# Kernel optimization log

Measured on AMD Instinct MI355X. Metric: run time of the kernel, lower is better.

The kernel has to match this reference:

```python
import jax, jax.numpy as jnp
import numpy as np

D_IN = 512
HLS = [1024, 1024, 512]
N_Q = 4096
N_K = 16384
N_CLASSES = 100
BN_EPS = 1e-5


def _bn(x, gamma, beta):
    # BatchNorm1d in training mode: per-batch mean/biased-var normalization
    m = jnp.mean(x, axis=0)
    v = jnp.var(x, axis=0)
    return gamma * (x - m) * jax.lax.rsqrt(v + BN_EPS) + beta


def _neg_cdist(a, b):
    # -||a_i - b_j||_2 via expanded form (GEMM-dominated)
    a2 = jnp.sum(a * a, axis=1, keepdims=True)          # [N,1]
    b2 = jnp.sum(b * b, axis=1, keepdims=True).T        # [1,M]
    d2 = a2 + b2 - 2.0 * (a @ b.T)                      # [N,M]
    return -jnp.sqrt(jnp.maximum(d2, 0.0))


def setup_inputs() -> dict:
    key = jax.random.key(0)
    ks = jax.random.split(key, 32)
    inp = {
        "x": jax.random.normal(ks[0], (N_Q, D_IN), jnp.float32),
        "x_n": jax.random.normal(ks[1], (N_K, D_IN), jnp.float32),
        "y_n": jax.random.randint(ks[2], (N_K,), 0, N_CLASSES, jnp.int32),
        "in_gamma": jnp.ones((D_IN,), jnp.float32),
        "in_beta": jnp.zeros((D_IN,), jnp.float32),
    }
    dims = [D_IN] + HLS
    ki = 3
    for i in range(len(HLS)):
        fan_in = dims[i]
        bound = 1.0 / np.sqrt(fan_in)
        inp[f"W{i}"] = jax.random.uniform(ks[ki], (dims[i + 1], dims[i]), jnp.float32, -bound, bound); ki += 1
        inp[f"b{i}"] = jax.random.uniform(ks[ki], (dims[i + 1],), jnp.float32, -bound, bound); ki += 1
        inp[f"g{i}"] = jnp.ones((dims[i + 1],), jnp.float32)
        inp[f"bt{i}"] = jnp.zeros((dims[i + 1],), jnp.float32)
    return inp


def reference(x, x_n, y_n, in_gamma, in_beta,
              W0, b0, g0, bt0, W1, b1, g1, bt1, W2, b2, g2, bt2):
    x = _bn(x, in_gamma, in_beta)
    x_n = _bn(x_n, in_gamma, in_beta)
    layers = [(W0, b0, g0, bt0), (W1, b1, g1, bt1), (W2, b2, g2, bt2)]
    for W, b, g, bt in layers:
        x = _bn(jnp.tanh(x @ W.T + b), g, bt)
        x_n = _bn(jnp.tanh(x_n @ W.T + b), g, bt)
    sim = _neg_cdist(x, x_n)                       # [N_Q, N_K]
    scores = jax.nn.softmax(sim, axis=1)
    y_ohe = jax.nn.one_hot(y_n, N_CLASSES, dtype=x.dtype)  # [N_K, C]
    return jnp.clip(scores @ y_ohe, 0.0, 1.0)
```

## Files before the change

kernel.cpp:

```cpp
#include <hip/hip_runtime.h>
#include <math.h>

#define NQ 4096
#define NK 16384
#define NROWS 20480
#define NCLS 100
#define PCLS 112
#define DCH 16

typedef __attribute__((ext_vector_type(8))) short bf16x8;
typedef __attribute__((ext_vector_type(4))) float f32x4;

__device__ inline unsigned short f2bf(float f) {
  unsigned u = __float_as_uint(f);
  u += 0x7fff + ((u >> 16) & 1);
  return (unsigned short)(u >> 16);
}
__device__ inline void upk(unsigned u, float& a, float& b) {
  a = __uint_as_float(u << 16);
  b = __uint_as_float(u & 0xffff0000u);
}
__device__ inline float fast_tanh(float x) {
  float e = __expf(2.f * x);
  return 1.f - 2.f / (e + 1.f);
}
__device__ inline void gload_lds16(const unsigned short* g, unsigned short* l) {
  __builtin_amdgcn_global_load_lds(
      (const __attribute__((address_space(1))) unsigned int*)g,
      (__attribute__((address_space(3))) unsigned int*)l, 16, 0, 0);
}

__global__ __launch_bounds__(256) void conv_bf16(
    const float* __restrict__ in, unsigned short* __restrict__ outp, size_t n4) {
  size_t i = (size_t)blockIdx.x * 256 + threadIdx.x;
  size_t stride = (size_t)gridDim.x * 256;
  for (; i < n4; i += stride) {
    float4 v = ((const float4*)in)[i];
    unsigned lo = (unsigned)f2bf(v.x) | ((unsigned)f2bf(v.y) << 16);
    unsigned hi = (unsigned)f2bf(v.z) | ((unsigned)f2bf(v.w) << 16);
    ((uint2*)outp)[i] = make_uint2(lo, hi);
  }
}

__global__ __launch_bounds__(256) void colstats_part_f(
    const float* __restrict__ A, int D, int rpc, float* __restrict__ part) {
  int j = blockIdx.x * 256 + threadIdx.x;
  int c = blockIdx.y;
  const float* p = A + (size_t)c * rpc * D + j;
  float s = 0.f, s2 = 0.f;
#pragma unroll 4
  for (int r = 0; r < rpc; ++r) {
    float v = p[(size_t)r * D];
    s += v; s2 += v * v;
  }
  part[(size_t)c * 2 * D + j] = s;
  part[(size_t)c * 2 * D + D + j] = s2;
}

__global__ __launch_bounds__(256) void finish_ab(
    const float* __restrict__ part, int D, float invN,
    const float* __restrict__ g, const float* __restrict__ bt,
    float* __restrict__ ab) {
  int j = blockIdx.x * 256 + threadIdx.x;
  if (j >= D) return;
  float s = 0.f, s2 = 0.f;
  for (int c = 0; c < 64; ++c) {
    s += part[(size_t)c * 2 * D + j];
    s2 += part[(size_t)c * 2 * D + D + j];
  }
  float m = s * invN;
  float v = fmaxf(s2 * invN - m * m, 0.f);
  float a = g[j] * rsqrtf(v + 1e-5f);
  ab[2 * j] = a;
  ab[2 * j + 1] = bt[j] - a * m;
}

__global__ __launch_bounds__(256) void ab_from_stats(
    const float* __restrict__ st, const float* __restrict__ g,
    const float* __restrict__ bt, float invN, float* __restrict__ ab, int M) {
  int j = blockIdx.x * 256 + threadIdx.x;
  if (j >= M) return;
  float s = st[2 * j], s2 = st[2 * j + 1];
  float m = s * invN;
  float v = fmaxf(s2 * invN - m * m, 0.f);
  float a = g[j] * rsqrtf(v + 1e-5f);
  ab[2 * j] = a;
  ab[2 * j + 1] = bt[j] - a * m;
}

__global__ __launch_bounds__(256) void fold_w(
    const float* __restrict__ W, const float* __restrict__ b,
    const float* __restrict__ ab, int K,
    unsigned short* __restrict__ Wo, float* __restrict__ bo) {
  int j = blockIdx.x;
  int t = threadIdx.x;
  const float* Wr = W + (size_t)j * K;
  unsigned short* Wor = Wo + (size_t)j * K;
  float s = 0.f;
  for (int k = t; k < K; k += 256) {
    float w = Wr[k];
    Wor[k] = f2bf(ab[2 * k] * w);
    s += ab[2 * k + 1] * w;
  }
  __shared__ float red[4];
#pragma unroll
  for (int off = 32; off; off >>= 1) s += __shfl_down(s, off, 64);
  if ((t & 63) == 0) red[t >> 6] = s;
  __syncthreads();
  if (t == 0) bo[j] = b[j] + red[0] + red[1] + red[2] + red[3];
}

__global__ __launch_bounds__(256) void gemm_v5(
    const unsigned short* __restrict__ A, const unsigned short* __restrict__ W,
    const float* __restrict__ bias, unsigned short* __restrict__ C,
    float* __restrict__ st, int M, int K) {
  __shared__ unsigned short As[2][128 * 64];
  __shared__ unsigned short Ws[2][128 * 64];
  int tid = threadIdx.x;
  int l = tid & 63, w = tid >> 6;
  int rowBase = blockIdx.y * 128, colBase = blockIdx.x * 128;
  int rowOff = (w >> 1) * 64, colOff = (w & 1) * 64;
  int fr = l & 15, fc = l >> 4;

  const unsigned short* Ag[4];
  const unsigned short* Wg[4];
  int slot[4];
#pragma unroll
  for (int j = 0; j < 4; ++j) {
    int i = tid + j * 256;
    int r = i >> 3, c = (i & 7) ^ (r & 7);
    slot[j] = i * 8;
    Ag[j] = A + (size_t)(rowBase + r) * K + c * 8;
    Wg[j] = W + (size_t)(colBase + r) * K + c * 8;
  }
  auto stage = [&](int s, int bb) {
    int ko = s * 64;
#pragma unroll
    for (int j = 0; j < 4; ++j) {
      gload_lds16(Ag[j] + ko, &As[bb][0] + slot[j]);
      gload_lds16(Wg[j] + ko, &Ws[bb][0] + slot[j]);
    }
  };

  f32x4 acc[4][4];
#pragma unroll
  for (int m = 0; m < 4; ++m)
#pragma unroll
    for (int n = 0; n < 4; ++n) acc[m][n] = (f32x4){0.f, 0.f, 0.f, 0.f};

  int NS = K >> 6;
  stage(0, 0);
  __syncthreads();
  for (int s = 0; s < NS; ++s) {
    if (s + 1 < NS) stage(s + 1, (s + 1) & 1);
    int b = s & 1;
#pragma unroll
    for (int kc = 0; kc < 2; ++kc) {
      bf16x8 av[4], bv[4];
#pragma unroll
      for (int m = 0; m < 4; ++m) {
        int row = rowOff + m * 16 + fr;
        int sl = (kc * 4 + fc) ^ (row & 7);
        av[m] = *(const bf16x8*)((const char*)&As[b][0] + row * 128 + sl * 16);
      }
#pragma unroll
      for (int n = 0; n < 4; ++n) {
        int row = colOff + n * 16 + fr;
        int sl = (kc * 4 + fc) ^ (row & 7);
        bv[n] = *(const bf16x8*)((const char*)&Ws[b][0] + row * 128 + sl * 16);
      }
#pragma unroll
      for (int m = 0; m < 4; ++m)
#pragma unroll
        for (int n = 0; n < 4; ++n)
          acc[m][n] = __builtin_amdgcn_mfma_f32_16x16x32_bf16(av[m], bv[n], acc[m][n], 0, 0, 0);
    }
    __syncthreads();
  }

  float ts1[4] = {0.f, 0.f, 0.f, 0.f};
  float ts2[4] = {0.f, 0.f, 0.f, 0.f};
#pragma unroll
  for (int m = 0; m < 4; ++m) {
#pragma unroll
    for (int r = 0; r < 4; ++r) {
      size_t row = rowBase + rowOff + m * 16 + fc * 4 + r;
      unsigned short* Crow = C + row * M;
#pragma unroll
      for (int n = 0; n < 4; ++n) {
        int col = colBase + colOff + n * 16 + fr;
        float val = fast_tanh(acc[m][n][r] + bias[col]);
        Crow[col] = f2bf(val);
        ts1[n] += val;
        ts2[n] += val * val;
      }
    }
  }
#pragma unroll
  for (int n = 0; n < 4; ++n) {
    float s1 = ts1[n], s2 = ts2[n];
    s1 += __shfl_xor(s1, 16, 64); s1 += __shfl_xor(s1, 32, 64);
    s2 += __shfl_xor(s2, 16, 64); s2 += __shfl_xor(s2, 32, 64);
    if (fc == 0) {
      int col = colBase + colOff + n * 16 + fr;
      atomicAdd(&st[2 * col], s1);
      atomicAdd(&st[2 * col + 1], s2);
    }
  }
}

__global__ __launch_bounds__(256) void bn_final(
    unsigned short* __restrict__ F, const float* __restrict__ ab,
    float* __restrict__ norms) {
  int w = threadIdx.x >> 6, l = threadIdx.x & 63;
  int row = blockIdx.x * 4 + w;
  unsigned short* p = F + (size_t)row * 512 + l * 8;
  uint4 v = *(const uint4*)p;
  int j0 = l * 8;
  float f[8];
  upk(v.x, f[0], f[1]); upk(v.y, f[2], f[3]);
  upk(v.z, f[4], f[5]); upk(v.w, f[6], f[7]);
  float s = 0.f;
  unsigned pk[4];
#pragma unroll
  for (int e = 0; e < 8; e += 2) {
    float a0 = ab[2 * (j0 + e)] * f[e] + ab[2 * (j0 + e) + 1];
    float a1 = ab[2 * (j0 + e + 1)] * f[e + 1] + ab[2 * (j0 + e + 1) + 1];
    s += a0 * a0 + a1 * a1;
    pk[e >> 1] = (unsigned)f2bf(a0) | ((unsigned)f2bf(a1) << 16);
  }
  *(uint4*)p = make_uint4(pk[0], pk[1], pk[2], pk[3]);
#pragma unroll
  for (int off = 32; off; off >>= 1) s += __shfl_down(s, off, 64);
  if (l == 0) norms[row] = s;
}

__global__ __launch_bounds__(256) void scatter_ohe(
    const int* __restrict__ yn, unsigned short* __restrict__ oheT) {
  int k = blockIdx.x * 256 + threadIdx.x;
  if (k < NK) oheT[(size_t)yn[k] * NK + k] = 0x3F80;
}

__global__ __launch_bounds__(512, 2) void dist_v5(
    const unsigned short* __restrict__ F,
    const float* __restrict__ norms,
    const unsigned short* __restrict__ oheT,
    float* __restrict__ part) {
  __shared__ unsigned short kbuf[3][128 * 64];
  __shared__ unsigned short Qs[64 * 512];
  __shared__ unsigned short Ps[64][136];
  __shared__ float k2s[1024];
  int tid = threadIdx.x;
  int l = tid & 63, w = tid >> 6;
  int qBase = blockIdx.x * 64;
  int kBase0 = blockIdx.y * 1024;
  int mg = w & 1, ng = w >> 1;
  int qtw = w & 3, cth = w >> 2;
  int fr = l & 15, fc = l >> 4;

  for (int i = tid; i < 1024; i += 512) k2s[i] = norms[NQ + kBase0 + i];
  float q2r0 = norms[qBase + mg * 32 + fr];
  float q2r1 = norms[qBase + mg * 32 + 16 + fr];
  __builtin_amdgcn_sched_barrier(0);

#pragma unroll
  for (int j = 0; j < 8; ++j) {
    int i = tid + j * 512;
    int row = i >> 6, p = i & 63;
    int c = (p & ~7) | ((p & 7) ^ (row & 7));
    gload_lds16(F + (size_t)(qBase + row) * 512 + c * 8, Qs + i * 8);
  }

  int i0 = tid, i1 = tid + 512;
  int r0 = i0 >> 3, c0 = (i0 & 7) ^ (r0 & 7);
  int r1 = i1 >> 3, c1 = (i1 & 7) ^ (r1 & 7);
  auto stage = [&](int slice, int bb) {
    int kRow = kBase0 + (slice >> 3) * 128;
    int ko = (slice & 7) * 64;
    gload_lds16(F + (size_t)(NQ + kRow + r0) * 512 + ko + c0 * 8,
                &kbuf[bb][0] + i0 * 8);
    gload_lds16(F + (size_t)(NQ + kRow + r1) * 512 + ko + c1 * 8,
                &kbuf[bb][0] + i1 * 8);
  };

  f32x4 accC[4];
#pragma unroll
  for (int c = 0; c < 4; ++c) accC[c] = (f32x4){0.f, 0.f, 0.f, 0.f};

  stage(0, 0);
  stage(1, 1);
  asm volatile("s_waitcnt lgkmcnt(0)" ::: "memory");

  for (int kt = 0; kt < 8; ++kt) {
    f32x4 acc[2][2];
#pragma unroll
    for (int t2 = 0; t2 < 2; ++t2)
#pragma unroll
      for (int qt = 0; qt < 2; ++qt) acc[t2][qt] = (f32x4){0.f, 0.f, 0.f, 0.f};
    bf16x8 ob[4][4];
#pragma unroll
    for (int kc = 0; kc < 4; ++kc)
#pragma unroll
      for (int c = 0; c < 4; ++c) ob[kc][c] = (bf16x8){0, 0, 0, 0, 0, 0, 0, 0};
#pragma unroll
    for (int s = 0; s < 8; ++s) {
      int slice = kt * 8 + s;
      if (slice == 63) {
        asm volatile("s_waitcnt vmcnt(0)" ::: "memory");
      } else if (s == 1 || s == 2) {
        asm volatile("s_waitcnt vmcnt(18)" ::: "memory");
      } else {
        asm volatile("s_waitcnt vmcnt(2)" ::: "memory");
      }
      __builtin_amdgcn_s_barrier();
      __builtin_amdgcn_sched_barrier(0);
      int b = slice % 3;
      bf16x8 kv[2][2];
#pragma unroll
      for (int kc = 0; kc < 2; ++kc)
#pragma unroll
        for (int t2 = 0; t2 < 2; ++t2) {
          int row = ng * 32 + t2 * 16 + fr;
          int sl = (kc * 4 + fc) ^ (row & 7);
          kv[kc][t2] = *(const bf16x8*)((const char*)&kbuf[b][0] + row * 128 + sl * 16);
        }
      bf16x8 avx[2][2];
#pragma unroll
      for (int kc = 0; kc < 2; ++kc)
#pragma unroll
        for (int qt = 0; qt < 2; ++qt) {
          int C = (s * 2 + kc) * 4 + fc;
          int p = (C & ~7) | ((C & 7) ^ (fr & 7));
          int row = mg * 32 + qt * 16 + fr;
          avx[kc][qt] = *(const bf16x8*)((const char*)Qs + row * 1024 + p * 16);
        }
      if (slice + 2 < 64) stage(slice + 2, (slice + 2) % 3);
      if (s == 0) {
        __builtin_amdgcn_sched_barrier(0);
#pragma unroll
        for (int kc = 0; kc < 4; ++kc)
#pragma unroll
          for (int c = 0; c < 4; ++c) {
            int ctg = cth * 4 + c;
            if (ctg < 7)
              ob[kc][c] = *(const bf16x8*)(
                  oheT + (size_t)(ctg * 16 + fr) * NK + kBase0 + kt * 128 + kc * 32 + fc * 8);
          }
        __builtin_amdgcn_sched_barrier(0);
      }
#pragma unroll
      for (int kc = 0; kc < 2; ++kc)
#pragma unroll
        for (int t2 = 0; t2 < 2; ++t2)
#pragma unroll
          for (int qt = 0; qt < 2; ++qt)
            acc[t2][qt] = __builtin_amdgcn_mfma_f32_16x16x32_bf16(
                kv[kc][t2], avx[kc][qt], acc[t2][qt], 0, 0, 0);
    }
#pragma unroll
    for (int t2 = 0; t2 < 2; ++t2) {
      float k2v[4];
#pragma unroll
      for (int r = 0; r < 4; ++r)
        k2v[r] = k2s[kt * 128 + ng * 32 + t2 * 16 + fc * 4 + r];
#pragma unroll
      for (int qt = 0; qt < 2; ++qt) {
        int q = mg * 32 + qt * 16 + fr;
        float q2 = qt ? q2r1 : q2r0;
        float pv[4];
#pragma unroll
        for (int r = 0; r < 4; ++r) {
          float d2 = q2 + k2v[r] - 2.f * acc[t2][qt][r];
          pv[r] = __expf(-sqrtf(fmaxf(d2, 0.f)));
        }
        unsigned lo = (unsigned)f2bf(pv[0]) | ((unsigned)f2bf(pv[1]) << 16);
        unsigned hi = (unsigned)f2bf(pv[2]) | ((unsigned)f2bf(pv[3]) << 16);
        *(uint2*)(&Ps[q][ng * 32 + t2 * 16 + fc * 4]) = make_uint2(lo, hi);
      }
    }
    asm volatile("s_waitcnt lgkmcnt(0)" ::: "memory");
    __builtin_amdgcn_s_barrier();
    __builtin_amdgcn_sched_barrier(0);
#pragma unroll
    for (int kc = 0; kc < 4; ++kc) {
      bf16x8 pa = *(const bf16x8*)(&Ps[qtw * 16 + fr][kc * 32 + fc * 8]);
#pragma unroll
      for (int c = 0; c < 4; ++c) {
        int ctg = cth * 4 + c;
        if (ctg < 7)
          accC[c] = __builtin_amdgcn_mfma_f32_16x16x32_bf16(pa, ob[kc][c], accC[c], 0, 0, 0);
      }
    }
  }
#pragma unroll
  for (int c = 0; c < 4; ++c) {
    int ctg = cth * 4 + c;
    if (ctg < 7) {
#pragma unroll
      for (int r = 0; r < 4; ++r) {
        int q = qBase + qtw * 16 + fc * 4 + r;
        part[((size_t)q * DCH + blockIdx.y) * PCLS + ctg * 16 + fr] = accC[c][r];
      }
    }
  }
}

__global__ __launch_bounds__(128) void combine_out(
    const float* __restrict__ part, float* __restrict__ outp) {
  int q = blockIdx.x;
  int t = threadIdx.x;
  float num = 0.f;
  if (t < NCLS) {
#pragma unroll
    for (int ch = 0; ch < DCH; ++ch)
      num += part[((size_t)q * DCH + ch) * PCLS + t];
  }
  __shared__ float sn[128];
  sn[t] = (t < NCLS) ? num : 0.f;
  __syncthreads();
#pragma unroll
  for (int off = 64; off; off >>= 1) {
    if (t < off) sn[t] += sn[t + off];
    __syncthreads();
  }
  float L = sn[0];
  if (t < NCLS) outp[(size_t)q * NCLS + t] = fminf(fmaxf(num / L, 0.f), 1.f);
}

extern "C" void kernel_launch(void* const* d_in, const int* in_sizes, int n_in,
                              void* d_out, int out_size, void* d_ws, size_t ws_size,
                              hipStream_t stream) {
  (void)in_sizes; (void)n_in; (void)out_size; (void)ws_size;
  const float* x   = (const float*)d_in[0];
  const float* xn  = (const float*)d_in[1];
  const int*   yn  = (const int*)d_in[2];
  const float* ing = (const float*)d_in[3];
  const float* inb = (const float*)d_in[4];
  const float* Wl[3]  = {(const float*)d_in[5], (const float*)d_in[9],  (const float*)d_in[13]};
  const float* bl[3]  = {(const float*)d_in[6], (const float*)d_in[10], (const float*)d_in[14]};
  const float* gl[3]  = {(const float*)d_in[7], (const float*)d_in[11], (const float*)d_in[15]};
  const float* btl[3] = {(const float*)d_in[8], (const float*)d_in[12], (const float*)d_in[16]};
  float* outp = (float*)d_out;

  unsigned short* featA = (unsigned short*)d_ws;
  unsigned short* featB = featA + (size_t)NROWS * 1024;
  unsigned short* wq  = featB + (size_t)NROWS * 1024;
  unsigned short* wk  = wq + (size_t)1024 * 1024;
  unsigned short* ohe = wk + (size_t)1024 * 1024;
  float* spart = (float*)(ohe + (size_t)PCLS * NK);
  float* abq   = spart + 64 * 2 * 512;
  float* abk   = abq + 2048;
  float* statq = abk + 2048;
  float* statk = statq + 2048;
  float* bpq   = statk + 2048;
  float* bpk   = bpq + 1024;
  float* norms = bpk + 1024;
  float* part  = norms + NROWS;

  colstats_part_f<<<dim3(2, 64), 256, 0, stream>>>(x, 512, NQ / 64, spart);
  finish_ab<<<2, 256, 0, stream>>>(spart, 512, 1.0f / NQ, ing, inb, abq);
  colstats_part_f<<<dim3(2, 64), 256, 0, stream>>>(xn, 512, NK / 64, spart);
  finish_ab<<<2, 256, 0, stream>>>(spart, 512, 1.0f / NK, ing, inb, abk);

  conv_bf16<<<1024, 256, 0, stream>>>(x, featA, (size_t)NQ * 512 / 4);
  conv_bf16<<<2048, 256, 0, stream>>>(xn, featA + (size_t)NQ * 512, (size_t)NK * 512 / 4);

  hipMemsetAsync(ohe, 0, (size_t)PCLS * NK * sizeof(unsigned short), stream);
  scatter_ohe<<<NK / 256, 256, 0, stream>>>(yn, ohe);

  int dims[4] = {512, 1024, 1024, 512};
  unsigned short *src = featA, *dst = featB;
  for (int lyr = 0; lyr < 3; ++lyr) {
    int K = dims[lyr], M = dims[lyr + 1];
    fold_w<<<M, 256, 0, stream>>>(Wl[lyr], bl[lyr], abq, K, wq, bpq);
    fold_w<<<M, 256, 0, stream>>>(Wl[lyr], bl[lyr], abk, K, wk, bpk);
    hipMemsetAsync(statq, 0, (size_t)M * 2 * sizeof(float), stream);
    hipMemsetAsync(statk, 0, (size_t)M * 2 * sizeof(float), stream);
    gemm_v5<<<dim3(M / 128, NQ / 128), 256, 0, stream>>>(src, wq, bpq, dst, statq, M, K);
    gemm_v5<<<dim3(M / 128, NK / 128), 256, 0, stream>>>(
        src + (size_t)NQ * K, wk, bpk, dst + (size_t)NQ * M, statk, M, K);
    ab_from_stats<<<M / 256, 256, 0, stream>>>(statq, gl[lyr], btl[lyr], 1.0f / NQ, abq, M);
    ab_from_stats<<<M / 256, 256, 0, stream>>>(statk, gl[lyr], btl[lyr], 1.0f / NK, abk, M);
    unsigned short* t = src; src = dst; dst = t;
  }
  bn_final<<<NQ / 4, 256, 0, stream>>>(src, abq, norms);
  bn_final<<<NK / 4, 256, 0, stream>>>(src + (size_t)NQ * 512, abk, norms + NQ);

  dist_v5<<<dim3(NQ / 64, DCH), 512, 0, stream>>>(src, norms, ohe, part);
  combine_out<<<NQ, 128, 0, stream>>>(part, outp);
}
```

Measured before the change: 569.0 us.

## Deepen GEMM pipeline to four K32 stages and retile Q buffer in distance kernel

The MLP GEMM switches from a 2-stage K=64 double buffer with full __syncthreads to a 4-buffer K=32 ring with three stages in flight. It uses explicit vmcnt waits and a single s_barrier per step, so global-to-LDS loads overlap more MFMA work. The distance kernel's query tile in LDS is regrouped into 64-column sub-tiles of 128-byte rows with an 8-way XOR swizzle, simplifying address math and possibly changing bank-conflict behaviour. The risks are halving MFMA work per barrier and depending on the exact vmcnt counts being correct for race-free reuse of the ring buffers.

```diff
diff --git a/kernel.cpp b/kernel.cpp
--- a/kernel.cpp
+++ b/kernel.cpp
@@ -110,33 +110,33 @@
   if (t == 0) bo[j] = b[j] + red[0] + red[1] + red[2] + red[3];
 }
 
-__global__ __launch_bounds__(256) void gemm_v5(
+__global__ __launch_bounds__(256) void gemm_v6(
     const unsigned short* __restrict__ A, const unsigned short* __restrict__ W,
     const float* __restrict__ bias, unsigned short* __restrict__ C,
     float* __restrict__ st, int M, int K) {
-  __shared__ unsigned short As[2][128 * 64];
-  __shared__ unsigned short Ws[2][128 * 64];
+  __shared__ unsigned short As[4][128 * 32];
+  __shared__ unsigned short Ws[4][128 * 32];
   int tid = threadIdx.x;
   int l = tid & 63, w = tid >> 6;
   int rowBase = blockIdx.y * 128, colBase = blockIdx.x * 128;
   int rowOff = (w >> 1) * 64, colOff = (w & 1) * 64;
   int fr = l & 15, fc = l >> 4;
 
-  const unsigned short* Ag[4];
-  const unsigned short* Wg[4];
-  int slot[4];
-#pragma unroll
-  for (int j = 0; j < 4; ++j) {
+  const unsigned short* Ag[2];
+  const unsigned short* Wg[2];
+  int slot[2];
+#pragma unroll
+  for (int j = 0; j < 2; ++j) {
     int i = tid + j * 256;
-    int r = i >> 3, c = (i & 7) ^ (r & 7);
+    int r = i >> 2, c = (i & 3) ^ (r & 3);
     slot[j] = i * 8;
     Ag[j] = A + (size_t)(rowBase + r) * K + c * 8;
     Wg[j] = W + (size_t)(colBase + r) * K + c * 8;
   }
   auto stage = [&](int s, int bb) {
-    int ko = s * 64;
-#pragma unroll
-    for (int j = 0; j < 4; ++j) {
+    int ko = s * 32;
+#pragma unroll
+    for (int j = 0; j < 2; ++j) {
       gload_lds16(Ag[j] + ko, &As[bb][0] + slot[j]);
       gload_lds16(Wg[j] + ko, &Ws[bb][0] + slot[j]);
     }
@@ -148,34 +148,40 @@
 #pragma unroll
     for (int n = 0; n < 4; ++n) acc[m][n] = (f32x4){0.f, 0.f, 0.f, 0.f};
 
-  int NS = K >> 6;
+  int NS = K >> 5;
   stage(0, 0);
-  __syncthreads();
+  stage(1, 1);
+  stage(2, 2);
   for (int s = 0; s < NS; ++s) {
-    if (s + 1 < NS) stage(s + 1, (s + 1) & 1);
-    int b = s & 1;
-#pragma unroll
-    for (int kc = 0; kc < 2; ++kc) {
-      bf16x8 av[4], bv[4];
-#pragma unroll
-      for (int m = 0; m < 4; ++m) {
-        int row = rowOff + m * 16 + fr;
-        int sl = (kc * 4 + fc) ^ (row & 7);
-        av[m] = *(const bf16x8*)((const char*)&As[b][0] + row * 128 + sl * 16);
-      }
-#pragma unroll
-      for (int n = 0; n < 4; ++n) {
-        int row = colOff + n * 16 + fr;
-        int sl = (kc * 4 + fc) ^ (row & 7);
-        bv[n] = *(const bf16x8*)((const char*)&Ws[b][0] + row * 128 + sl * 16);
-      }
-#pragma unroll
-      for (int m = 0; m < 4; ++m)
-#pragma unroll
-        for (int n = 0; n < 4; ++n)
-          acc[m][n] = __builtin_amdgcn_mfma_f32_16x16x32_bf16(av[m], bv[n], acc[m][n], 0, 0, 0);
-    }
-    __syncthreads();
+    if (s + 2 < NS) {
+      asm volatile("s_waitcnt vmcnt(8)" ::: "memory");
+    } else if (s + 1 < NS) {
+      asm volatile("s_waitcnt vmcnt(4)" ::: "memory");
+    } else {
+      asm volatile("s_waitcnt vmcnt(0)" ::: "memory");
+    }
+    __builtin_amdgcn_s_barrier();
+    __builtin_amdgcn_sched_barrier(0);
+    int b = s & 3;
+    bf16x8 av[4], bv[4];
+#pragma unroll
+    for (int m = 0; m < 4; ++m) {
+      int row = rowOff + m * 16 + fr;
+      int p = fc ^ (row & 3);
+      av[m] = *(const bf16x8*)((const char*)&As[b][0] + row * 64 + p * 16);
+    }
+#pragma unroll
+    for (int n = 0; n < 4; ++n) {
+      int row = colOff + n * 16 + fr;
+      int p = fc ^ (row & 3);
+      bv[n] = *(const bf16x8*)((const char*)&Ws[b][0] + row * 64 + p * 16);
+    }
+    if (s + 3 < NS) stage(s + 3, (s + 3) & 3);
+#pragma unroll
+    for (int m = 0; m < 4; ++m)
+#pragma unroll
+      for (int n = 0; n < 4; ++n)
+        acc[m][n] = __builtin_amdgcn_mfma_f32_16x16x32_bf16(av[m], bv[n], acc[m][n], 0, 0, 0);
   }
 
   float ts1[4] = {0.f, 0.f, 0.f, 0.f};
@@ -247,7 +253,7 @@
     const unsigned short* __restrict__ oheT,
     float* __restrict__ part) {
   __shared__ unsigned short kbuf[3][128 * 64];
-  __shared__ unsigned short Qs[64 * 512];
+  __shared__ unsigned short Qs[8 * 64 * 64];
   __shared__ unsigned short Ps[64][136];
   __shared__ float k2s[1024];
   int tid = threadIdx.x;
@@ -266,9 +272,10 @@
 #pragma unroll
   for (int j = 0; j < 8; ++j) {
     int i = tid + j * 512;
-    int row = i >> 6, p = i & 63;
-    int c = (p & ~7) | ((p & 7) ^ (row & 7));
-    gload_lds16(F + (size_t)(qBase + row) * 512 + c * 8, Qs + i * 8);
+    int ss = i >> 9;
+    int row = (i >> 3) & 63;
+    int c = (i & 7) ^ (row & 7);
+    gload_lds16(F + (size_t)(qBase + row) * 512 + ss * 64 + c * 8, Qs + i * 8);
   }
 
   int i0 = tid, i1 = tid + 512;
@@ -329,10 +336,9 @@
       for (int kc = 0; kc < 2; ++kc)
 #pragma unroll
         for (int qt = 0; qt < 2; ++qt) {
-          int C = (s * 2 + kc) * 4 + fc;
-          int p = (C & ~7) | ((C & 7) ^ (fr & 7));
           int row = mg * 32 + qt * 16 + fr;
-          avx[kc][qt] = *(const bf16x8*)((const char*)Qs + row * 1024 + p * 16);
+          int sl = (kc * 4 + fc) ^ (fr & 7);
+          avx[kc][qt] = *(const bf16x8*)((const char*)Qs + s * 8192 + row * 128 + sl * 16);
         }
       if (slice + 2 < 64) stage(slice + 2, (slice + 2) % 3);
       if (s == 0) {
@@ -476,8 +482,8 @@
     fold_w<<<M, 256, 0, stream>>>(Wl[lyr], bl[lyr], abk, K, wk, bpk);
     hipMemsetAsync(statq, 0, (size_t)M * 2 * sizeof(float), stream);
     hipMemsetAsync(statk, 0, (size_t)M * 2 * sizeof(float), stream);
-    gemm_v5<<<dim3(M / 128, NQ / 128), 256, 0, stream>>>(src, wq, bpq, dst, statq, M, K);
-    gemm_v5<<<dim3(M / 128, NK / 128), 256, 0, stream>>>(
+    gemm_v6<<<dim3(M / 128, NQ / 128), 256, 0, stream>>>(src, wq, bpq, dst, statq, M, K);
+    gemm_v6<<<dim3(M / 128, NK / 128), 256, 0, stream>>>(
         src + (size_t)NQ * K, wk, bpk, dst + (size_t)NQ * M, statk, M, K);
     ab_from_stats<<<M / 256, 256, 0, stream>>>(statq, gl[lyr], btl[lyr], 1.0f / NQ, abq, M);
     ab_from_stats<<<M / 256, 256, 0, stream>>>(statk, gl[lyr], btl[lyr], 1.0f / NK, abk, M);
```

Result: no change. 566.2 us (-0.5%).
